# Kernel optimization log

Measured on AMD Instinct MI355X. Metric: run time of the kernel, lower is better.

The kernel has to match this reference:

```python
import jax, jax.numpy as jnp
import numpy as np
from jax.scipy.special import logsumexp

S, D, K, R, P = 500, 768, 16, 256, 64  # seq_len, bert_dim, out_dim, n_pairs, max wordpieces/entity


def setup_inputs() -> dict:
    key = jax.random.key(0)
    k1, k2, k3, k4, k5, k6 = jax.random.split(key, 6)
    word_embeddings = jax.random.normal(k1, (S, D), jnp.float32)
    # kaiming_normal_ fan_in = D*K (last two dims collapsed); gain sqrt(2) for relu
    W = jax.random.normal(k2, (D, K, D), jnp.float32) * np.float32((2.0 / (K * D)) ** 0.5)
    idx1 = jax.random.randint(k3, (R, P), 0, S)
    idx2 = jax.random.randint(k4, (R, P), 0, S)
    # ragged mention lengths -> padding masks (at least 1 valid wordpiece)
    len1 = jax.random.randint(k5, (R,), 1, P + 1)
    len2 = jax.random.randint(k6, (R,), 1, P + 1)
    pos = jnp.arange(P)
    mask1 = (pos[None, :] < len1[:, None]).astype(jnp.float32)
    mask2 = (pos[None, :] < len2[:, None]).astype(jnp.float32)
    return {"word_embeddings": word_embeddings, "W": W, "idx1": idx1, "idx2": idx2,
            "mask1": mask1, "mask2": mask2}


def reference(word_embeddings, W, idx1, idx2, mask1, mask2):
    # gather ragged mention wordpieces (padded to P per entity)
    e1 = word_embeddings[idx1]  # [R, P, D]
    e2 = word_embeddings[idx2]  # [R, P, D]
    # biaffine: z[r,k,p,q] = e1[r,p,:] @ W[:,k,:] @ e2[r,q,:]
    zh = jnp.einsum('rpd,dke->rpke', e1, W)      # [R, P, K, D]
    z = jnp.einsum('rpke,rqe->rkpq', zh, e2)     # [R, K, P, P]
    # logsumexp pooling over all valid (p, q) mention-token pairs
    b = mask1[:, None, :, None] * mask2[:, None, None, :]  # [R, 1, P, P]
    scores = logsumexp(z, axis=(2, 3), b=b)      # [R, K]
    return scores
```

## Files before the change

### kernel.cpp

```cpp
#include <hip/hip_runtime.h>
#include <math.h>

#define S_ 500
#define D_ 768
#define K_ 16
#define R_ 256
#define P_ 64

typedef unsigned short ushort_t;
typedef __attribute__((ext_vector_type(8))) short short8;
typedef __attribute__((ext_vector_type(4))) float floatx4;

__device__ inline ushort_t f2bf(float x) {
  unsigned int u = __float_as_uint(x);
  u += 0x7fffu + ((u >> 16) & 1u);
  return (ushort_t)(u >> 16);
}

#define GLD_LDS16(g, l)                                                        \
  __builtin_amdgcn_global_load_lds(                                            \
      (const __attribute__((address_space(1))) void*)(g),                      \
      (__attribute__((address_space(3))) void*)(l), 16, 0, 0)

__global__ __launch_bounds__(256) void prep(const float* __restrict__ WE,
                                            const float* __restrict__ W,
                                            ushort_t* __restrict__ WEb,
                                            ushort_t* __restrict__ Wt) {
  const int t = threadIdx.x;
  if (blockIdx.x < 384) {
    int gid = blockIdx.x * 256 + t;
    int row = gid / 192;
    ushort4 o = {0, 0, 0, 0};
    if (row < S_) {
      float4 v = *(const float4*)(WE + (size_t)gid * 4);
      o.x = f2bf(v.x); o.y = f2bf(v.y); o.z = f2bf(v.z); o.w = f2bf(v.w);
    }
    *(ushort4*)(WEb + (size_t)gid * 4) = o;
    return;
  }
  __shared__ float tile[64][68];
  const int tb = blockIdx.x - 384;
  const int n0 = (tb % 192) * 64, d0 = (tb / 192) * 64;
  {
    const int r = t >> 2, cbase = (t & 3) * 16;
#pragma unroll
    for (int i = 0; i < 4; i++) {
      float4 v = *(const float4*)(W + (size_t)(d0 + r) * 12288 + n0 + cbase + i * 4);
      *(float4*)&tile[r][cbase + i * 4] = v;
    }
  }
  __syncthreads();
  {
    const int bc = t & 15;
    const int br4 = (t >> 4) * 4;
    float4 tv[4];
#pragma unroll
    for (int ii = 0; ii < 4; ii++)
      tv[ii] = *(const float4*)&tile[bc * 4 + ii][br4];
#pragma unroll
    for (int j = 0; j < 4; j++) {
      ushort4 o;
      o.x = f2bf(((const float*)&tv[0])[j]);
      o.y = f2bf(((const float*)&tv[1])[j]);
      o.z = f2bf(((const float*)&tv[2])[j]);
      o.w = f2bf(((const float*)&tv[3])[j]);
      *(ushort4*)(Wt + (size_t)(n0 + br4 + j) * 768 + d0 + bc * 4) = o;
    }
  }
}

template <int MODE>
__global__ __launch_bounds__(256) void mm_bt(const ushort_t* __restrict__ A,
                                             const ushort_t* __restrict__ Bm,
                                             void* __restrict__ Cout) {
  __shared__ ushort_t As[128 * 32];
  __shared__ ushort_t Bs[128 * 32];
  const int tid = threadIdx.x;
  const int wave = tid >> 6, lane = tid & 63;
  const int m0 = blockIdx.y * 128, n0 = blockIdx.x * 128;
  const int wm = (wave & 1) * 64, wn = (wave >> 1) * 64;
  const int col = lane & 15, quad = lane >> 4;

  floatx4 acc[4][4];
#pragma unroll
  for (int i = 0; i < 4; i++)
#pragma unroll
    for (int j = 0; j < 4; j++)
#pragma unroll
      for (int e = 0; e < 4; e++) acc[i][j][e] = 0.f;

  const int srow = wave * 32 + (lane >> 2);
  const int scol = (lane & 3) * 8;

  for (int k0 = 0; k0 < D_; k0 += 32) {
    const ushort_t* ga = A + (size_t)(m0 + srow) * D_ + k0 + scol;
    const ushort_t* gb = Bm + (size_t)(n0 + srow) * D_ + k0 + scol;
    __syncthreads();
    GLD_LDS16(ga, &As[(wave * 32) * 32]);
    GLD_LDS16(ga + 16 * D_, &As[(wave * 32 + 16) * 32]);
    GLD_LDS16(gb, &Bs[(wave * 32) * 32]);
    GLD_LDS16(gb + 16 * D_, &Bs[(wave * 32 + 16) * 32]);
    __syncthreads();

    short8 a[4], b[4];
#pragma unroll
    for (int i = 0; i < 4; i++)
      a[i] = *(const short8*)&As[(wm + i * 16 + col) * 32 + quad * 8];
#pragma unroll
    for (int j = 0; j < 4; j++)
      b[j] = *(const short8*)&Bs[(wn + j * 16 + col) * 32 + quad * 8];
#pragma unroll
    for (int i = 0; i < 4; i++)
#pragma unroll
      for (int j = 0; j < 4; j++) {
        if (MODE == 0)
          acc[i][j] = __builtin_amdgcn_mfma_f32_16x16x32_bf16(b[j], a[i], acc[i][j], 0, 0, 0);
        else
          acc[i][j] = __builtin_amdgcn_mfma_f32_16x16x32_bf16(a[i], b[j], acc[i][j], 0, 0, 0);
      }
  }

  if (MODE == 0) {
    ushort_t* C = (ushort_t*)Cout;
#pragma unroll
    for (int i = 0; i < 4; i++) {
      int m = m0 + wm + i * 16 + col;
#pragma unroll
      for (int j = 0; j < 4; j++) {
        int n = n0 + wn + j * 16 + quad * 4;
        ushort4 o;
        o.x = f2bf(acc[i][j][0]); o.y = f2bf(acc[i][j][1]);
        o.z = f2bf(acc[i][j][2]); o.w = f2bf(acc[i][j][3]);
        *(ushort4*)(C + (size_t)m * 12288 + n) = o;
      }
    }
  } else {
    float* G = (float*)Cout;
#pragma unroll
    for (int i = 0; i < 4; i++) {
      int s1 = (m0 + wm + i * 16) >> 4;
#pragma unroll
      for (int j = 0; j < 4; j++) {
        int s2 = n0 + wn + j * 16 + col;
        if (s1 < S_ && s2 < S_)
          *(floatx4*)(G + (((size_t)s1 * S_ + s2) << 4) + quad * 4) = acc[i][j];
      }
    }
  }
}

__global__ __launch_bounds__(256) void lse_part(const float* __restrict__ G,
                                                const int* __restrict__ idx1,
                                                const int* __restrict__ idx2,
                                                const float* __restrict__ mask1,
                                                const float* __restrict__ mask2,
                                                float* __restrict__ pm,
                                                float* __restrict__ ps) {
  const int r = blockIdx.x >> 2, seg = blockIdx.x & 3;
  const int tid = threadIdx.x;
  __shared__ int b1[P_], b2[P_];
  __shared__ int s_len1, s_len2;
  __shared__ float wmx[4][K_], wsum[4][K_];

  if (tid < 64) {
    float mv = mask1[r * P_ + tid];
    unsigned long long bal = __ballot(mv > 0.5f);
    if (tid == 0) s_len1 = (int)__popcll(bal);
    b1[tid] = idx1[r * P_ + tid] * (S_ * K_);
  } else if (tid < 128) {
    int q = tid - 64;
    float mv = mask2[r * P_ + q];
    unsigned long long bal = __ballot(mv > 0.5f);
    if (q == 0) s_len2 = (int)__popcll(bal);
    b2[q] = idx2[r * P_ + q] * K_;
  }
  __syncthreads();
  const int len2 = s_len2;
  const int total = s_len1 * len2;

  float m[K_], s[K_];
#pragma unroll
  for (int k = 0; k < K_; k++) { m[k] = -3.0e38f; s[k] = 0.f; }

  for (int i = seg * 256 + tid; i < total; i += 1024) {
    int p = i / len2;
    int q = i - p * len2;
    const float4* g4 = (const float4*)(G + b1[p] + b2[q]);
    float4 z0 = g4[0], z1 = g4[1], z2 = g4[2], z3 = g4[3];
    float z[K_] = {z0.x, z0.y, z0.z, z0.w, z1.x, z1.y, z1.z, z1.w,
                   z2.x, z2.y, z2.z, z2.w, z3.x, z3.y, z3.z, z3.w};
#pragma unroll
    for (int k = 0; k < K_; k++) {
      float zk = z[k];
      float M2 = fmaxf(m[k], zk);
      s[k] = s[k] * __expf(m[k] - M2) + __expf(zk - M2);
      m[k] = M2;
    }
  }

#pragma unroll
  for (int off = 1; off < 64; off <<= 1) {
#pragma unroll
    for (int k = 0; k < K_; k++) {
      float mo = __shfl_xor(m[k], off, 64);
      float so = __shfl_xor(s[k], off, 64);
      float M2 = fmaxf(m[k], mo);
      s[k] = s[k] * __expf(m[k] - M2) + so * __expf(mo - M2);
      m[k] = M2;
    }
  }
  const int wave = tid >> 6, lane = tid & 63;
  if (lane == 0) {
#pragma unroll
    for (int k = 0; k < K_; k++) { wmx[wave][k] = m[k]; wsum[wave][k] = s[k]; }
  }
  __syncthreads();
  if (tid < K_) {
    float M = -3.0e38f, Ssum = 0.f;
#pragma unroll
    for (int w = 0; w < 4; w++) {
      float mo = wmx[w][tid], so = wsum[w][tid];
      float M2 = fmaxf(M, mo);
      Ssum = Ssum * __expf(M - M2) + so * __expf(mo - M2);
      M = M2;
    }
    pm[(r * 4 + seg) * K_ + tid] = M;
    ps[(r * 4 + seg) * K_ + tid] = Ssum;
  }
}

__global__ __launch_bounds__(256) void lse_combine(const float* __restrict__ pm,
                                                   const float* __restrict__ ps,
                                                   float* __restrict__ out) {
  int gid = blockIdx.x * 256 + threadIdx.x;
  int r = gid >> 4, k = gid & 15;
  float M = -3.0e38f, Ssum = 0.f;
#pragma unroll
  for (int seg = 0; seg < 4; seg++) {
    float mo = pm[(r * 4 + seg) * K_ + k];
    float so = ps[(r * 4 + seg) * K_ + k];
    float M2 = fmaxf(M, mo);
    Ssum = Ssum * __expf(M - M2) + so * __expf(mo - M2);
    M = M2;
  }
  out[gid] = M + __logf(Ssum);
}

extern "C" void kernel_launch(void* const* d_in, const int* in_sizes, int n_in,
                              void* d_out, int out_size, void* d_ws, size_t ws_size,
                              hipStream_t stream) {
  const float* WE    = (const float*)d_in[0];
  const float* W     = (const float*)d_in[1];
  const int*   idx1  = (const int*)d_in[2];
  const int*   idx2  = (const int*)d_in[3];
  const float* mask1 = (const float*)d_in[4];
  const float* mask2 = (const float*)d_in[5];
  float* out = (float*)d_out;

  ushort_t* WEb   = (ushort_t*)d_ws;
  ushort_t* Wt    = WEb + (size_t)512 * 768;
  ushort_t* projb = Wt + (size_t)12288 * 768;
  float*    G     = (float*)(projb + (size_t)8192 * 768);
  float*    pm    = G + (size_t)S_ * S_ * K_;
  float*    ps    = pm + R_ * 4 * K_;

  prep<<<384 + 2304, 256, 0, stream>>>(WE, W, WEb, Wt);
  mm_bt<0><<<dim3(96, 4), 256, 0, stream>>>(WEb, Wt, (void*)projb);
  mm_bt<1><<<dim3(4, 64), 256, 0, stream>>>(projb, WEb, (void*)G);
  lse_part<<<R_ * 4, 256, 0, stream>>>(G, idx1, idx2, mask1, mask2, pm, ps);
  lse_combine<<<16, 256, 0, stream>>>(pm, ps, out);
}
```

Baseline: 152.7 us.

## Double-buffer GEMM K-loop with async LDS loads and store G as bf16

Rewrites the mm_bt main loop to prefetch the next 64-wide K tile into a second LDS buffer while computing on the current one. Synchronization now uses explicit vmcnt waits and raw s_barrier instead of two __syncthreads per step. Separately, the pairwise score tensor G is written as bf16 instead of fp32, which halves its write traffic and the gather traffic in lse_part. The bf16 rounding of the logits adds precision loss before logsumexp, and the larger LDS footprint may reduce occupancy.

```diff
diff --git a/kernel.cpp b/kernel.cpp
--- a/kernel.cpp
+++ b/kernel.cpp
@@ -6,6 +6,7 @@
 #define K_ 16
 #define R_ 256
 #define P_ 64
+#define NT 12
 
 typedef unsigned short ushort_t;
 typedef __attribute__((ext_vector_type(8))) short short8;
@@ -21,6 +22,10 @@
   __builtin_amdgcn_global_load_lds(                                            \
       (const __attribute__((address_space(1))) void*)(g),                      \
       (__attribute__((address_space(3))) void*)(l), 16, 0, 0)
+
+#define ASM_BARRIER asm volatile("s_barrier" ::: "memory")
+#define WAIT_VM8 asm volatile("s_waitcnt vmcnt(8)" ::: "memory")
+#define WAIT_VM0 asm volatile("s_waitcnt vmcnt(0)" ::: "memory")
 
 __global__ __launch_bounds__(256) void prep(const float* __restrict__ WE,
                                             const float* __restrict__ W,
@@ -73,8 +78,8 @@
 __global__ __launch_bounds__(256) void mm_bt(const ushort_t* __restrict__ A,
                                              const ushort_t* __restrict__ Bm,
                                              void* __restrict__ Cout) {
-  __shared__ ushort_t As[128 * 32];
-  __shared__ ushort_t Bs[128 * 32];
+  __shared__ ushort_t As[2][2][128 * 32];
+  __shared__ ushort_t Bs[2][2][128 * 32];
   const int tid = threadIdx.x;
   const int wave = tid >> 6, lane = tid & 63;
   const int m0 = blockIdx.y * 128, n0 = blockIdx.x * 128;
@@ -91,34 +96,56 @@
 
   const int srow = wave * 32 + (lane >> 2);
   const int scol = (lane & 3) * 8;
-
-  for (int k0 = 0; k0 < D_; k0 += 32) {
-    const ushort_t* ga = A + (size_t)(m0 + srow) * D_ + k0 + scol;
-    const ushort_t* gb = Bm + (size_t)(n0 + srow) * D_ + k0 + scol;
-    __syncthreads();
-    GLD_LDS16(ga, &As[(wave * 32) * 32]);
-    GLD_LDS16(ga + 16 * D_, &As[(wave * 32 + 16) * 32]);
-    GLD_LDS16(gb, &Bs[(wave * 32) * 32]);
-    GLD_LDS16(gb + 16 * D_, &Bs[(wave * 32 + 16) * 32]);
-    __syncthreads();
-
-    short8 a[4], b[4];
-#pragma unroll
-    for (int i = 0; i < 4; i++)
-      a[i] = *(const short8*)&As[(wm + i * 16 + col) * 32 + quad * 8];
-#pragma unroll
-    for (int j = 0; j < 4; j++)
-      b[j] = *(const short8*)&Bs[(wn + j * 16 + col) * 32 + quad * 8];
-#pragma unroll
-    for (int i = 0; i < 4; i++)
-#pragma unroll
-      for (int j = 0; j < 4; j++) {
-        if (MODE == 0)
-          acc[i][j] = __builtin_amdgcn_mfma_f32_16x16x32_bf16(b[j], a[i], acc[i][j], 0, 0, 0);
-        else
-          acc[i][j] = __builtin_amdgcn_mfma_f32_16x16x32_bf16(a[i], b[j], acc[i][j], 0, 0, 0);
-      }
-  }
+  const ushort_t* ga0 = A + (size_t)(m0 + srow) * D_ + scol;
+  const ushort_t* gb0 = Bm + (size_t)(n0 + srow) * D_ + scol;
+  const int ldsbase = (wave * 32) * 32;
+
+#define ISSUE_TILE(t_, buf_)                                                   \
+  do {                                                                         \
+    const ushort_t* ga = ga0 + (t_)*64;                                        \
+    const ushort_t* gb = gb0 + (t_)*64;                                        \
+    GLD_LDS16(ga, &As[buf_][0][ldsbase]);                                      \
+    GLD_LDS16(ga + 16 * D_, &As[buf_][0][ldsbase + 16 * 32]);                  \
+    GLD_LDS16(ga + 32, &As[buf_][1][ldsbase]);                                 \
+    GLD_LDS16(ga + 32 + 16 * D_, &As[buf_][1][ldsbase + 16 * 32]);             \
+    GLD_LDS16(gb, &Bs[buf_][0][ldsbase]);                                      \
+    GLD_LDS16(gb + 16 * D_, &Bs[buf_][0][ldsbase + 16 * 32]);                  \
+    GLD_LDS16(gb + 32, &Bs[buf_][1][ldsbase]);                                 \
+    GLD_LDS16(gb + 32 + 16 * D_, &Bs[buf_][1][ldsbase + 16 * 32]);             \
+  } while (0)
+
+  ISSUE_TILE(0, 0);
+  for (int t = 0; t < NT; ++t) {
+    const int cur = t & 1;
+    if (t + 1 < NT) {
+      ISSUE_TILE(t + 1, cur ^ 1);
+      WAIT_VM8;
+    } else {
+      WAIT_VM0;
+    }
+    ASM_BARRIER;
+#pragma unroll
+    for (int s = 0; s < 2; ++s) {
+      short8 a[4], b[4];
+#pragma unroll
+      for (int i = 0; i < 4; i++)
+        a[i] = *(const short8*)&As[cur][s][(wm + i * 16 + col) * 32 + quad * 8];
+#pragma unroll
+      for (int j = 0; j < 4; j++)
+        b[j] = *(const short8*)&Bs[cur][s][(wn + j * 16 + col) * 32 + quad * 8];
+#pragma unroll
+      for (int i = 0; i < 4; i++)
+#pragma unroll
+        for (int j = 0; j < 4; j++) {
+          if (MODE == 0)
+            acc[i][j] = __builtin_amdgcn_mfma_f32_16x16x32_bf16(b[j], a[i], acc[i][j], 0, 0, 0);
+          else
+            acc[i][j] = __builtin_amdgcn_mfma_f32_16x16x32_bf16(a[i], b[j], acc[i][j], 0, 0, 0);
+        }
+    }
+    ASM_BARRIER;
+  }
+#undef ISSUE_TILE
 
   if (MODE == 0) {
     ushort_t* C = (ushort_t*)Cout;
@@ -135,21 +162,25 @@
       }
     }
   } else {
-    float* G = (float*)Cout;
+    ushort_t* G = (ushort_t*)Cout;
 #pragma unroll
     for (int i = 0; i < 4; i++) {
       int s1 = (m0 + wm + i * 16) >> 4;
 #pragma unroll
       for (int j = 0; j < 4; j++) {
         int s2 = n0 + wn + j * 16 + col;
-        if (s1 < S_ && s2 < S_)
-          *(floatx4*)(G + (((size_t)s1 * S_ + s2) << 4) + quad * 4) = acc[i][j];
+        if (s1 < S_ && s2 < S_) {
+          ushort4 o;
+          o.x = f2bf(acc[i][j][0]); o.y = f2bf(acc[i][j][1]);
+          o.z = f2bf(acc[i][j][2]); o.w = f2bf(acc[i][j][3]);
+          *(ushort4*)(G + (((size_t)s1 * S_ + s2) << 4) + quad * 4) = o;
+        }
       }
     }
   }
 }
 
-__global__ __launch_bounds__(256) void lse_part(const float* __restrict__ G,
+__global__ __launch_bounds__(256) void lse_part(const ushort_t* __restrict__ G,
                                                 const int* __restrict__ idx1,
                                                 const int* __restrict__ idx2,
                                                 const float* __restrict__ mask1,
@@ -185,10 +216,15 @@
   for (int i = seg * 256 + tid; i < total; i += 1024) {
     int p = i / len2;
     int q = i - p * len2;
-    const float4* g4 = (const float4*)(G + b1[p] + b2[q]);
-    float4 z0 = g4[0], z1 = g4[1], z2 = g4[2], z3 = g4[3];
-    float z[K_] = {z0.x, z0.y, z0.z, z0.w, z1.x, z1.y, z1.z, z1.w,
-                   z2.x, z2.y, z2.z, z2.w, z3.x, z3.y, z3.z, z3.w};
+    const uint4* g4 = (const uint4*)(G + b1[p] + b2[q]);
+    uint4 w0 = g4[0], w1 = g4[1];
+    unsigned int uu[8] = {w0.x, w0.y, w0.z, w0.w, w1.x, w1.y, w1.z, w1.w};
+    float z[K_];
+#pragma unroll
+    for (int h = 0; h < 8; h++) {
+      z[2 * h + 0] = __uint_as_float(uu[h] << 16);
+      z[2 * h + 1] = __uint_as_float(uu[h] & 0xffff0000u);
+    }
 #pragma unroll
     for (int k = 0; k < K_; k++) {
       float zk = z[k];
@@ -260,8 +296,8 @@
   ushort_t* WEb   = (ushort_t*)d_ws;
   ushort_t* Wt    = WEb + (size_t)512 * 768;
   ushort_t* projb = Wt + (size_t)12288 * 768;
-  float*    G     = (float*)(projb + (size_t)8192 * 768);
-  float*    pm    = G + (size_t)S_ * S_ * K_;
+  ushort_t* G     = projb + (size_t)8192 * 768;
+  float*    pm    = (float*)(G + (size_t)S_ * S_ * K_);
   float*    ps    = pm + R_ * 4 * K_;
 
   prep<<<384 + 2304, 256, 0, stream>>>(WE, W, WEb, Wt);
```

Result: faster. 143.8 us (-5.8%).
